# Optimization experiments

Hardware: AMD Instinct MI355X
Metric: run time of the kernel (lower is better)

Reference implementation:

```python
import jax, jax.numpy as jnp
import numpy as np

B, T, D_IN, H1, H2 = 32, 2048, 1024, 512, 32


def setup_inputs() -> dict:
    key = jax.random.key(0)
    ks = jax.random.split(key, 8)
    avf_out = jax.random.normal(ks[0], (B, T, D_IN), dtype=jnp.float32)
    # seq_len in [1, T] so every sample has a non-empty slice (matches torch usage)
    seq_len = jax.random.randint(ks[1], (B,), 1, T + 1, dtype=jnp.int32)
    s = 0.02
    W1 = jax.random.normal(ks[2], (D_IN, H1), dtype=jnp.float32) * s
    b1 = jnp.zeros((H1,), dtype=jnp.float32)
    W2 = jax.random.normal(ks[3], (H1, H2), dtype=jnp.float32) * s
    b2 = jnp.zeros((H2,), dtype=jnp.float32)
    W3 = jax.random.normal(ks[4], (H2, 1), dtype=jnp.float32) * s
    b3 = jnp.zeros((1,), dtype=jnp.float32)
    return {"avf_out": avf_out, "W1": W1, "b1": b1, "W2": W2, "b2": b2,
            "W3": W3, "b3": b3, "seq_len": seq_len}


def reference(avf_out, W1, b1, W2, b2, W3, b3, seq_len):
    h = jax.nn.relu(jnp.einsum('btd,dh->bth', avf_out, W1) + b1)
    h = jnp.einsum('bth,hk->btk', h, W2) + b2
    logits = jax.nn.sigmoid(jnp.einsum('btk,ko->bto', h, W3) + b3)[..., 0]  # [B, T]
    # ragged per-sample top-k (k = seq_len//16 + 1 over first seq_len entries) + mean,
    # vectorized via masked descending sort + cumsum (no per-sample loop)
    Tn = logits.shape[1]
    valid = jnp.arange(Tn)[None, :] < seq_len[:, None]            # [B, T]
    NEG = jnp.float32(-1.0)  # below sigmoid range, so padded slots never enter top-k
    masked = jnp.where(valid, logits, NEG)
    sorted_desc = -jnp.sort(-masked, axis=1)                      # [B, T] descending
    csum = jnp.cumsum(sorted_desc, axis=1)
    k = seq_len // 16 + 1                                         # k <= seq_len always
    topk_sum = jnp.take_along_axis(csum, (k - 1)[:, None].astype(jnp.int32), axis=1)[:, 0]
    return topk_sum / k.astype(logits.dtype)                      # [B]
```

## Files before the change

kernel.cpp:

```cpp
#include <hip/hip_runtime.h>

typedef __bf16 bf16;
typedef __bf16 bf16x4 __attribute__((ext_vector_type(4)));
typedef __bf16 bf16x8 __attribute__((ext_vector_type(8)));
typedef float f32x4 __attribute__((ext_vector_type(4)));

#define K_TOT 1024
#define N_TOT 512
#define T_SEQ 2048
#define NB 32

__device__ __forceinline__ void async16(const void* g, void* l) {
    __builtin_amdgcn_global_load_lds(
        (const __attribute__((address_space(1))) unsigned int*)g,
        (__attribute__((address_space(3))) unsigned int*)l, 16, 0, 0);
}

__global__ __launch_bounds__(256) void transpose_prep(
        const float* __restrict__ W1, bf16* __restrict__ W1T,
        const float* __restrict__ W2, const float* __restrict__ b2,
        const float* __restrict__ W3, const float* __restrict__ b3,
        const int* __restrict__ seq_len,
        float* __restrict__ v, int* __restrict__ tiles, int* __restrict__ done) {
    __shared__ float tile[32][33];
    __shared__ int nb2[32], off2[32];
    const int t = threadIdx.x;
    const int k0 = blockIdx.x * 32;
    const int n0 = blockIdx.y * 32;
#pragma unroll
    for (int p = 0; p < 4; p++) {
        int kl = p * 8 + (t >> 5);
        int nl = t & 31;
        tile[kl][nl] = W1[(k0 + kl) * 512 + n0 + nl];
    }
    __syncthreads();
#pragma unroll
    for (int p = 0; p < 4; p++) {
        int nl = p * 8 + (t >> 5);
        int kl = t & 31;
        W1T[(n0 + nl) * 1024 + k0 + kl] = (bf16)tile[kl][nl];
    }

    if (blockIdx.x == 0 && blockIdx.y == 0) {
        for (int h = t; h < 512; h += 256) {
            float s = 0.f;
#pragma unroll
            for (int c = 0; c < 32; c++) s += W2[h * 32 + c] * W3[c];
            v[h] = s;
        }
        if (t == 0) {
            float cc = b3[0];
            for (int c = 0; c < 32; c++) cc += b2[c] * W3[c];
            v[512] = cc;
        }
        if (t < 32) {
            nb2[t] = (seq_len[t] + 127) >> 7;
            done[t] = 0;
        }
        __syncthreads();
        if (t == 0) {
            int a = 0;
            for (int i = 0; i < 32; i++) { off2[i] = a; a += nb2[i]; }
            tiles[0] = a;
        }
        __syncthreads();
        for (int idx = t; idx < 512; idx += 256) {
            int b = idx >> 4, j = idx & 15;
            if (j < nb2[b]) tiles[1 + off2[b] + j] = idx;
        }
    }
}

__device__ __forceinline__ int sw_idx(int row, int e) {
    return row * 64 + (((e >> 3) ^ (row & 7)) << 3) + (e & 7);
}

__global__ __launch_bounds__(512, 2) void gemm_fused(const float* __restrict__ A,
                                                     const bf16* __restrict__ W1T,
                                                     const float* __restrict__ b1,
                                                     const float* __restrict__ v,
                                                     const int* __restrict__ tiles,
                                                     const int* __restrict__ seq_len,
                                                     int* __restrict__ done,
                                                     float* __restrict__ logits,
                                                     float* __restrict__ out) {
    __shared__ bf16 smem[2][(128 + 512) * 64];

    const int nact = tiles[0];
    if ((int)blockIdx.x >= nact) return;
    const int tileid = tiles[1 + blockIdx.x];
    const int m0 = tileid * 128;
    const int bsmp = tileid >> 4;

    const int t = threadIdx.x;
    const int wave = t >> 6, lane = t & 63;
    const int q = lane >> 4, l15 = lane & 15;
    const int wm = wave >> 2, wn = wave & 3;

    const int arow = t >> 2, ac = t & 3;
    const float* agp = A + (size_t)(m0 + arow) * K_TOT + ac * 4;

    const int bl_row = wave * 64 + (lane >> 3);
    const int bl_chunk = (lane & 7) ^ ((lane >> 3) & 7);
    const bf16* bgp = W1T + (size_t)bl_row * K_TOT + bl_chunk * 8;

    f32x4 acc[4][8] = {};
    float4 av[4];

    auto loadA = [&](int k0) {
#pragma unroll
        for (int p = 0; p < 4; p++) av[p] = *(const float4*)(agp + k0 + p * 16);
    };
    auto asyncB = [&](int k0, int b) {
        bf16* bs = smem[b] + 128 * 64;
#pragma unroll
        for (int j = 0; j < 8; j++)
            async16(bgp + k0 + (size_t)j * 8 * K_TOT, bs + (wave * 64 + j * 8) * 64);
    };
    auto writeA = [&](int b) {
        bf16* as = smem[b];
#pragma unroll
        for (int p = 0; p < 4; p++) {
            bf16x4 w;
            w[0] = (bf16)av[p].x; w[1] = (bf16)av[p].y;
            w[2] = (bf16)av[p].z; w[3] = (bf16)av[p].w;
            int chunk = 2 * p + (ac >> 1);
            int idx = arow * 64 + ((chunk ^ (arow & 7)) << 3) + (ac & 1) * 4;
            *(bf16x4*)(&as[idx]) = w;
        }
    };
    auto mfma_phase = [&](int b) {
        const bf16* as = smem[b];
        const bf16* bs = smem[b] + 128 * 64;
#pragma unroll
        for (int kk = 0; kk < 64; kk += 32) {
            const int e = kk + q * 8;
            bf16x8 af[4], bfv[8];
#pragma unroll
            for (int mi = 0; mi < 4; mi++)
                af[mi] = *(const bf16x8*)(&as[sw_idx(wm * 64 + mi * 16 + l15, e)]);
#pragma unroll
            for (int ni = 0; ni < 8; ni++)
                bfv[ni] = *(const bf16x8*)(&bs[sw_idx(wn * 128 + ni * 16 + l15, e)]);
#pragma unroll
            for (int mi = 0; mi < 4; mi++)
#pragma unroll
                for (int ni = 0; ni < 8; ni++)
                    acc[mi][ni] = __builtin_amdgcn_mfma_f32_16x16x32_bf16(
                        af[mi], bfv[ni], acc[mi][ni], 0, 0, 0);
        }
    };

    loadA(0);
    asyncB(0, 0);
    writeA(0);
    __syncthreads();

#pragma unroll 1
    for (int k = 0; k < 16; k++) {
        const int buf = k & 1, nxt = buf ^ 1;
        if (k < 15) {
            loadA((k + 1) * 64);
            asyncB((k + 1) * 64, nxt);
        }
        mfma_phase(buf);
        if (k < 15) writeA(nxt);
        __syncthreads();
    }

    float bb[8], vv[8];
#pragma unroll
    for (int ni = 0; ni < 8; ni++) {
        int col = wn * 128 + ni * 16 + l15;
        bb[ni] = b1[col];
        vv[ni] = v[col];
    }
    const float cconst = v[512];

    __syncthreads();
    float* part = (float*)smem;

#pragma unroll
    for (int mi = 0; mi < 4; mi++) {
#pragma unroll
        for (int r = 0; r < 4; r++) {
            float s = 0.f;
#pragma unroll
            for (int ni = 0; ni < 8; ni++)
                s += fmaxf(acc[mi][ni][r] + bb[ni], 0.f) * vv[ni];
            s += __shfl_xor(s, 1);
            s += __shfl_xor(s, 2);
            s += __shfl_xor(s, 4);
            s += __shfl_xor(s, 8);
            if (l15 == 0) {
                int row = wm * 64 + mi * 16 + q * 4 + r;
                part[row * 4 + wn] = s;
            }
        }
    }
    __syncthreads();
    if (t < 128) {
        float s = part[t * 4] + part[t * 4 + 1] + part[t * 4 + 2] + part[t * 4 + 3] + cconst;
        logits[m0 + t] = 1.f / (1.f + __expf(-s));
    }

    const int L = seq_len[bsmp];
    const int nb = (L + 127) >> 7;

    float* vals  = (float*)smem;
    int*   redi  = (int*)(vals + 2048);
    unsigned* mnx = (unsigned*)(redi + 16);
    float* redf  = (float*)(mnx + 16);
    int*   wflag = (int*)(redf + 8);

    __syncthreads();
    if (t == 0) {
        __threadfence();
        int old = atomicAdd(&done[bsmp], 1);
        int win = (old == nb - 1);
        if (win) __threadfence();
        *wflag = win;
    }
    __syncthreads();
    if (!*wflag) return;

    const int kk = (L >> 4) + 1;
    const float* p = logits + bsmp * T_SEQ;

    unsigned mn = 0x3f800000u, mx = 0u;
    for (int i = t; i < L; i += 512) {
        float x = p[i];
        vals[i] = x;
        unsigned u = __float_as_uint(x);
        mn = min(mn, u); mx = max(mx, u);
    }
#pragma unroll
    for (int m = 32; m >= 1; m >>= 1) {
        mn = min(mn, (unsigned)__shfl_xor((int)mn, m));
        mx = max(mx, (unsigned)__shfl_xor((int)mx, m));
    }
    if (lane == 0) { mnx[wave] = mn; mnx[8 + wave] = mx; }
    __syncthreads();
    unsigned lo = mnx[0], hi = mnx[8];
#pragma unroll
    for (int w8 = 1; w8 < 8; w8++) {
        lo = min(lo, mnx[w8]); hi = max(hi, mnx[8 + w8]);
    }
    __syncthreads();

    int rb = 0;
    while (lo < hi) {
        unsigned w = hi - lo;
        unsigned t1 = w / 3u + 1u;
        unsigned m1 = lo + t1;
        unsigned m2 = lo + (w - w / 3u);
        if (m2 < m1) m2 = m1;
        float f1 = __uint_as_float(m1), f2 = __uint_as_float(m2);
        int c1 = 0, c2 = 0;
        for (int i = t; i < L; i += 512) {
            float x = vals[i];
            c1 += (x >= f1) ? 1 : 0;
            c2 += (x >= f2) ? 1 : 0;
        }
        int packed = (c1 << 12) | c2;
#pragma unroll
        for (int m = 32; m >= 1; m >>= 1) packed += __shfl_xor(packed, m);
        if (lane == 0) redi[(rb & 1) * 8 + wave] = packed;
        __syncthreads();
        int tot = 0;
#pragma unroll
        for (int w8 = 0; w8 < 8; w8++) tot += redi[(rb & 1) * 8 + w8];
        int C2 = tot & 0xFFF, C1 = tot >> 12;
        if (C2 >= kk)      { lo = m2; }
        else if (C1 >= kk) { lo = m1; hi = m2 - 1; }
        else               { hi = m1 - 1; }
        rb++;
    }
    const float thr = __uint_as_float(lo);

    int cg = 0; float sg = 0.f;
    for (int i = t; i < L; i += 512) {
        float x = vals[i];
        if (x > thr) { cg += 1; sg += x; }
    }
#pragma unroll
    for (int m = 32; m >= 1; m >>= 1) {
        cg += __shfl_xor(cg, m);
        sg += __shfl_xor(sg, m);
    }
    if (lane == 0) { redi[(rb & 1) * 8 + wave] = cg; redf[wave] = sg; }
    __syncthreads();
    if (t == 0) {
        int cgt = 0; float sgt = 0.f;
#pragma unroll
        for (int w8 = 0; w8 < 8; w8++) { cgt += redi[(rb & 1) * 8 + w8]; sgt += redf[w8]; }
        out[bsmp] = (sgt + (float)(kk - cgt) * thr) / (float)kk;
    }
}

extern "C" void kernel_launch(void* const* d_in, const int* in_sizes, int n_in,
                              void* d_out, int out_size, void* d_ws, size_t ws_size,
                              hipStream_t stream) {
    const float* avf = (const float*)d_in[0];
    const float* W1  = (const float*)d_in[1];
    const float* b1  = (const float*)d_in[2];
    const float* W2  = (const float*)d_in[3];
    const float* b2  = (const float*)d_in[4];
    const float* W3  = (const float*)d_in[5];
    const float* b3  = (const float*)d_in[6];
    const int* seq_len = (const int*)d_in[7];
    float* out = (float*)d_out;

    char* ws = (char*)d_ws;
    bf16*  W1T    = (bf16*)ws;
    float* v      = (float*)(ws + (1 << 20));
    int*   tiles  = (int*)(ws + (1 << 20) + 4096);
    int*   done   = (int*)(ws + (1 << 20) + 8192);
    float* logits = (float*)(ws + (1 << 20) + 12288);

    transpose_prep<<<dim3(32, 16), 256, 0, stream>>>(W1, W1T, W2, b2, W3, b3,
                                                     seq_len, v, tiles, done);
    gemm_fused<<<512, 512, 0, stream>>>(avf, W1T, b1, v, tiles, seq_len, done,
                                        logits, out);
}
```

Before: 411.6 us.

## Enlarge GEMM M-tile to 160 rows with single-buffered A tile

Raises the rows per workgroup from 128 to 160 so each W1 B-tile loaded into LDS is reused across more rows, and cuts the number of tiles per sample. The A tile becomes single-buffered with an extra barrier per k-step so that LDS fits the larger tile plus double-buffered B. Edge tiles clamp out-of-range row reads and mask logit writes. The costs are more accumulator registers, a second sync per iteration, and a coarser tail where partial tiles waste more work.

```diff
diff --git a/kernel.cpp b/kernel.cpp
--- a/kernel.cpp
+++ b/kernel.cpp
@@ -9,6 +9,9 @@
 #define N_TOT 512
 #define T_SEQ 2048
 #define NB 32
+#define M_TILE 160
+#define MAX_J 13
+#define ROW_MAX (NB * T_SEQ - 1)
 
 __device__ __forceinline__ void async16(const void* g, void* l) {
     __builtin_amdgcn_global_load_lds(
@@ -54,7 +57,7 @@
             v[512] = cc;
         }
         if (t < 32) {
-            nb2[t] = (seq_len[t] + 127) >> 7;
+            nb2[t] = (seq_len[t] + M_TILE - 1) / M_TILE;
             done[t] = 0;
         }
         __syncthreads();
@@ -66,7 +69,7 @@
         __syncthreads();
         for (int idx = t; idx < 512; idx += 256) {
             int b = idx >> 4, j = idx & 15;
-            if (j < nb2[b]) tiles[1 + off2[b] + j] = idx;
+            if (j < nb2[b]) tiles[1 + off2[b] + j] = (b << 4) | j;
         }
     }
 }
@@ -84,88 +87,103 @@
                                                      int* __restrict__ done,
                                                      float* __restrict__ logits,
                                                      float* __restrict__ out) {
-    __shared__ bf16 smem[2][(128 + 512) * 64];
+    __shared__ bf16 smem[M_TILE * 64 + 2 * N_TOT * 64];
+    bf16* As = smem;
+    bf16* Bs0 = smem + M_TILE * 64;
+    bf16* Bs1 = Bs0 + N_TOT * 64;
 
     const int nact = tiles[0];
     if ((int)blockIdx.x >= nact) return;
     const int tileid = tiles[1 + blockIdx.x];
-    const int m0 = tileid * 128;
     const int bsmp = tileid >> 4;
+    const int jj = tileid & 15;
+    const int m0 = bsmp * T_SEQ + jj * M_TILE;
 
     const int t = threadIdx.x;
     const int wave = t >> 6, lane = t & 63;
     const int q = lane >> 4, l15 = lane & 15;
     const int wm = wave >> 2, wn = wave & 3;
 
-    const int arow = t >> 2, ac = t & 3;
-    const float* agp = A + (size_t)(m0 + arow) * K_TOT + ac * 4;
+    const int c16 = t & 15, r0 = t >> 4;
+    const float* agp[5];
+#pragma unroll
+    for (int p = 0; p < 5; p++) {
+        int grow = m0 + r0 + p * 32;
+        if (grow > ROW_MAX) grow = ROW_MAX;
+        agp[p] = A + (size_t)grow * K_TOT + c16 * 4;
+    }
 
     const int bl_row = wave * 64 + (lane >> 3);
     const int bl_chunk = (lane & 7) ^ ((lane >> 3) & 7);
     const bf16* bgp = W1T + (size_t)bl_row * K_TOT + bl_chunk * 8;
 
-    f32x4 acc[4][8] = {};
-    float4 av[4];
+    f32x4 acc[5][8] = {};
+    float4 av[5];
 
     auto loadA = [&](int k0) {
 #pragma unroll
-        for (int p = 0; p < 4; p++) av[p] = *(const float4*)(agp + k0 + p * 16);
+        for (int p = 0; p < 5; p++) av[p] = *(const float4*)(agp[p] + k0);
     };
-    auto asyncB = [&](int k0, int b) {
-        bf16* bs = smem[b] + 128 * 64;
+    auto asyncB = [&](int k0, bf16* bs) {
 #pragma unroll
         for (int j = 0; j < 8; j++)
             async16(bgp + k0 + (size_t)j * 8 * K_TOT, bs + (wave * 64 + j * 8) * 64);
     };
-    auto writeA = [&](int b) {
-        bf16* as = smem[b];
-#pragma unroll
-        for (int p = 0; p < 4; p++) {
+    auto writeA = [&]() {
+#pragma unroll
+        for (int p = 0; p < 5; p++) {
             bf16x4 w;
             w[0] = (bf16)av[p].x; w[1] = (bf16)av[p].y;
             w[2] = (bf16)av[p].z; w[3] = (bf16)av[p].w;
-            int chunk = 2 * p + (ac >> 1);
-            int idx = arow * 64 + ((chunk ^ (arow & 7)) << 3) + (ac & 1) * 4;
-            *(bf16x4*)(&as[idx]) = w;
+            int row = r0 + p * 32;
+            int chunk = c16 >> 1;
+            int idx = row * 64 + ((chunk ^ (row & 7)) << 3) + (c16 & 1) * 4;
+            *(bf16x4*)(&As[idx]) = w;
         }
     };
-    auto mfma_phase = [&](int b) {
-        const bf16* as = smem[b];
-        const bf16* bs = smem[b] + 128 * 64;
+    auto mfma_phase = [&](const bf16* bs) {
 #pragma unroll
         for (int kk = 0; kk < 64; kk += 32) {
             const int e = kk + q * 8;
-            bf16x8 af[4], bfv[8];
-#pragma unroll
-            for (int mi = 0; mi < 4; mi++)
-                af[mi] = *(const bf16x8*)(&as[sw_idx(wm * 64 + mi * 16 + l15, e)]);
-#pragma unroll
-            for (int ni = 0; ni < 8; ni++)
-                bfv[ni] = *(const bf16x8*)(&bs[sw_idx(wn * 128 + ni * 16 + l15, e)]);
-#pragma unroll
-            for (int mi = 0; mi < 4; mi++)
-#pragma unroll
-                for (int ni = 0; ni < 8; ni++)
-                    acc[mi][ni] = __builtin_amdgcn_mfma_f32_16x16x32_bf16(
-                        af[mi], bfv[ni], acc[mi][ni], 0, 0, 0);
+            bf16x8 af[5];
+#pragma unroll
+            for (int mi = 0; mi < 5; mi++)
+                af[mi] = *(const bf16x8*)(&As[sw_idx(wm * 80 + mi * 16 + l15, e)]);
+#pragma unroll
+            for (int nh = 0; nh < 8; nh += 4) {
+                bf16x8 bfv[4];
+#pragma unroll
+                for (int ni = 0; ni < 4; ni++)
+                    bfv[ni] = *(const bf16x8*)(&bs[sw_idx(wn * 128 + (nh + ni) * 16 + l15, e)]);
+#pragma unroll
+                for (int mi = 0; mi < 5; mi++)
+#pragma unroll
+                    for (int ni = 0; ni < 4; ni++)
+                        acc[mi][nh + ni] = __builtin_amdgcn_mfma_f32_16x16x32_bf16(
+                            af[mi], bfv[ni], acc[mi][nh + ni], 0, 0, 0);
+            }
         }
     };
 
     loadA(0);
-    asyncB(0, 0);
-    writeA(0);
+    asyncB(0, Bs0);
+    writeA();
     __syncthreads();
 
 #pragma unroll 1
     for (int k = 0; k < 16; k++) {
-        const int buf = k & 1, nxt = buf ^ 1;
+        bf16* bcur = (k & 1) ? Bs1 : Bs0;
+        bf16* bnxt = (k & 1) ? Bs0 : Bs1;
         if (k < 15) {
             loadA((k + 1) * 64);
-            asyncB((k + 1) * 64, nxt);
-        }
-        mfma_phase(buf);
-        if (k < 15) writeA(nxt);
+            asyncB((k + 1) * 64, bnxt);
+        }
+        mfma_phase(bcur);
         __syncthreads();
+        if (k < 15) {
+            writeA();
+            __syncthreads();
+        }
     }
 
     float bb[8], vv[8];
@@ -177,11 +195,10 @@
     }
     const float cconst = v[512];
 
-    __syncthreads();
     float* part = (float*)smem;
 
 #pragma unroll
-    for (int mi = 0; mi < 4; mi++) {
+    for (int mi = 0; mi < 5; mi++) {
 #pragma unroll
         for (int r = 0; r < 4; r++) {
             float s = 0.f;
@@ -193,19 +210,19 @@
             s += __shfl_xor(s, 4);
             s += __shfl_xor(s, 8);
             if (l15 == 0) {
-                int row = wm * 64 + mi * 16 + q * 4 + r;
+                int row = wm * 80 + mi * 16 + q * 4 + r;
                 part[row * 4 + wn] = s;
             }
         }
     }
     __syncthreads();
-    if (t < 128) {
+    if (t < M_TILE && jj * M_TILE + t < T_SEQ) {
         float s = part[t * 4] + part[t * 4 + 1] + part[t * 4 + 2] + part[t * 4 + 3] + cconst;
         logits[m0 + t] = 1.f / (1.f + __expf(-s));
     }
 
     const int L = seq_len[bsmp];
-    const int nb = (L + 127) >> 7;
+    const int nb = (L + M_TILE - 1) / M_TILE;
 
     float* vals  = (float*)smem;
     int*   redi  = (int*)(vals + 2048);
@@ -320,6 +337,6 @@
 
     transpose_prep<<<dim3(32, 16), 256, 0, stream>>>(W1, W1T, W2, b2, W3, b3,
                                                      seq_len, v, tiles, done);
-    gemm_fused<<<512, 512, 0, stream>>>(avf, W1T, b1, v, tiles, seq_len, done,
-                                        logits, out);
-}
+    gemm_fused<<<NB * MAX_J, 512, 0, stream>>>(avf, W1T, b1, v, tiles, seq_len,
+                                               done, logits, out);
+}
```

After: 397.6 us. 3.4% less time.
